# Kernel optimization log

Measured on AMD Instinct MI355X. Metric: run time of the kernel, lower is better.

Reference implementation:

```python
import jax, jax.numpy as jnp
import numpy as np

D_MODEL = 1024
NUM_HEADS = 16
D_K = D_MODEL // NUM_HEADS


def setup_inputs() -> dict:
    key = jax.random.key(0)
    ks = jax.random.split(key, 9)
    B, S = 2, 2048
    s = 1.0 / np.sqrt(D_MODEL)
    return {
        "x": jax.random.normal(ks[0], (B, S, D_MODEL), dtype=jnp.float32),
        "Wq": jax.random.normal(ks[1], (D_MODEL, D_MODEL), dtype=jnp.float32) * s,
        "bq": jnp.zeros((D_MODEL,), dtype=jnp.float32),
        "Wk": jax.random.normal(ks[2], (D_MODEL, D_MODEL), dtype=jnp.float32) * s,
        "bk": jnp.zeros((D_MODEL,), dtype=jnp.float32),
        "Wv": jax.random.normal(ks[3], (D_MODEL, D_MODEL), dtype=jnp.float32) * s,
        "bv": jnp.zeros((D_MODEL,), dtype=jnp.float32),
        "Wo": jax.random.normal(ks[4], (D_MODEL, D_MODEL), dtype=jnp.float32) * s,
        "bo": jnp.zeros((D_MODEL,), dtype=jnp.float32),
    }


def reference(x, Wq, bq, Wk, bk, Wv, bv, Wo, bo):
    B, S, _ = x.shape
    # project and split heads: [B, H, S, d_k]
    def proj(W, b):
        return (x @ W + b).reshape(B, S, NUM_HEADS, D_K).transpose(0, 2, 1, 3)
    Q, K, V = proj(Wq, bq), proj(Wk, bk), proj(Wv, bv)
    scores = jnp.einsum("bhqd,bhkd->bhqk", Q, K) / jnp.sqrt(jnp.float32(D_K))
    causal = jnp.tril(jnp.ones((S, S), dtype=bool))
    scores = jnp.where(causal[None, None], scores, jnp.float32(-1e9))
    attn = jax.nn.softmax(scores, axis=-1)  # dropout=0 (eval)
    out = jnp.einsum("bhqk,bhkd->bhqd", attn, V)
    out = out.transpose(0, 2, 1, 3).reshape(B, S, D_MODEL)
    return out @ Wo + bo
```

## Files before the change

kernel.cpp:

```cpp
#include <hip/hip_runtime.h>

#define SEQ    2048
#define NH     16
#define DMODEL 1024

typedef __attribute__((ext_vector_type(4)))  float f32x4;
typedef __attribute__((ext_vector_type(8)))  short s16x8;
typedef __attribute__((ext_vector_type(4)))  short s16x4;
typedef __attribute__((ext_vector_type(2)))  unsigned u32x2;

__device__ __forceinline__ float bf2f(unsigned short u){
  union { unsigned int i; float f; } v; v.i = ((unsigned int)u) << 16; return v.f;
}
__device__ __forceinline__ unsigned short f2bf(float f){
  union { float f; unsigned int i; } v; v.f = f;
  unsigned int r = v.i + 0x7fffu + ((v.i >> 16) & 1u);
  return (unsigned short)(r >> 16);
}
__device__ __forceinline__ unsigned short f2bf_hu(float f){
  union { float f; unsigned int i; } v; v.f = f;
  return (unsigned short)((v.i + 0x8000u) >> 16);
}
__device__ __forceinline__ float fast_exp2(float x){
  return __builtin_amdgcn_exp2f(x);
}
__device__ __forceinline__ void gld_lds16(const void* g, void* l){
  __builtin_amdgcn_global_load_lds((const __attribute__((address_space(1))) void*)g,
                                   (__attribute__((address_space(3))) void*)l,
                                   16, 0, 0);
}
#define SB() __builtin_amdgcn_sched_barrier(0)

__global__ __launch_bounds__(256) void k_cast_x(const float* __restrict__ x,
                                                unsigned short* __restrict__ hi){
  int i = blockIdx.x * 256 + threadIdx.x;
  f32x4 v = ((const f32x4*)x)[i];
  s16x4 h;
  #pragma unroll
  for (int j = 0; j < 4; ++j) h[j] = (short)f2bf(v[j]);
  ((s16x4*)hi)[i] = h;
}

__global__ __launch_bounds__(256) void k_t_w(const float* __restrict__ W0,
                                             const float* __restrict__ W1,
                                             const float* __restrict__ W2,
                                             const float* __restrict__ W3,
                                             unsigned short* __restrict__ Wt){
  __shared__ float t[64][65];
  const float* Ws[4] = {W0, W1, W2, W3};
  const float* W = Ws[blockIdx.z];
  const int n0 = blockIdx.x * 64, k0 = blockIdx.y * 64;
  const int tid = threadIdx.x;
  #pragma unroll
  for (int i = 0; i < 16; ++i){
    int e = i * 256 + tid;
    int r = e >> 6, c = e & 63;
    t[r][c] = W[(size_t)(k0 + r) * 1024 + n0 + c];
  }
  __syncthreads();
  size_t base = ((size_t)blockIdx.z << 20);
  #pragma unroll
  for (int i = 0; i < 16; ++i){
    int e = i * 256 + tid;
    int nn = e >> 6, kk = e & 63;
    Wt[base + (size_t)(n0 + nn) * 1024 + k0 + kk] = f2bf(t[kk][nn]);
  }
}

__global__ __launch_bounds__(512, 2)
void gemm_qkv8(const unsigned short* __restrict__ A,
               const unsigned short* __restrict__ B,
               const float* __restrict__ bq, const float* __restrict__ bk,
               const float* __restrict__ bv,
               unsigned short* __restrict__ Qb, unsigned short* __restrict__ Kb,
               unsigned short* __restrict__ Vt)
{
  __shared__ __align__(16) unsigned short lA[2][256 * 64];
  __shared__ __align__(16) unsigned short lB[2][192 * 64];
  const int tid = threadIdx.x;
  const int lane = tid & 63, w = tid >> 6;
  const int wm = w >> 2, wn = w & 3;
  const int lr = lane & 15, lq = lane >> 4;
  const int m0 = blockIdx.y * 256, n0 = blockIdx.x * 192;

  size_t asrc[4]; unsigned adst[4];
  #pragma unroll
  for (int p = 0; p < 4; ++p){
    int c = p * 512 + tid;
    int row = c >> 3, lc = (c & 7) ^ (row & 7);
    asrc[p] = (size_t)(m0 + row) * 1024 + lc * 8;
    adst[p] = c * 8;
  }
  size_t bsrc[3]; unsigned bdst[3];
  #pragma unroll
  for (int p = 0; p < 3; ++p){
    int c = p * 512 + tid;
    int row = c >> 3, lc = (c & 7) ^ (row & 7);
    bsrc[p] = (size_t)(n0 + row) * 1024 + lc * 8;
    bdst[p] = c * 8;
  }
  auto stage = [&](int buf, int k0){
    #pragma unroll
    for (int p = 0; p < 4; ++p) gld_lds16(A + asrc[p] + k0, &lA[buf][adst[p]]);
    #pragma unroll
    for (int p = 0; p < 3; ++p) gld_lds16(B + bsrc[p] + k0, &lB[buf][bdst[p]]);
  };

  const int csw0 = ((0 + lq) ^ (lr & 7)) << 4;
  const int csw1 = ((4 + lq) ^ (lr & 7)) << 4;

  f32x4 acc[8][3];
  #pragma unroll
  for (int i = 0; i < 8; ++i)
    #pragma unroll
    for (int j = 0; j < 3; ++j) acc[i][j] = (f32x4)0.0f;

  stage(0, 0);
  stage(1, 64);
  asm volatile("s_waitcnt vmcnt(7)" ::: "memory");
  SB();
  __builtin_amdgcn_s_barrier();
  SB();

  for (int t = 0; t < 16; ++t){
    const int p = t & 1;
    s16x8 fa[8][2], fb[3][2];
    const char* baseA = (const char*)&lA[p][0];
    const char* baseB = (const char*)&lB[p][0];
    #pragma unroll
    for (int mf = 0; mf < 8; ++mf)
      fa[mf][0] = *(const s16x8*)(baseA + (wm * 128 + mf * 16 + lr) * 128 + csw0);
    #pragma unroll
    for (int nf = 0; nf < 3; ++nf)
      fb[nf][0] = *(const s16x8*)(baseB + (wn * 48 + nf * 16 + lr) * 128 + csw0);
    SB();
    #pragma unroll
    for (int mf = 0; mf < 8; ++mf)
      fa[mf][1] = *(const s16x8*)(baseA + (wm * 128 + mf * 16 + lr) * 128 + csw1);
    #pragma unroll
    for (int nf = 0; nf < 3; ++nf)
      fb[nf][1] = *(const s16x8*)(baseB + (wn * 48 + nf * 16 + lr) * 128 + csw1);
    asm volatile("s_waitcnt lgkmcnt(11)" ::: "memory");
    SB();
    #pragma unroll
    for (int mf = 0; mf < 8; ++mf)
      #pragma unroll
      for (int nf = 0; nf < 3; ++nf)
        acc[mf][nf] = __builtin_amdgcn_mfma_f32_16x16x32_bf16(fa[mf][0], fb[nf][0], acc[mf][nf], 0, 0, 0);
    SB();
    asm volatile("s_waitcnt lgkmcnt(0)" ::: "memory");
    SB();
    __builtin_amdgcn_s_barrier();
    SB();
    if (t + 2 < 16) stage(p, (t + 2) * 64);
    #pragma unroll
    for (int mf = 0; mf < 8; ++mf)
      #pragma unroll
      for (int nf = 0; nf < 3; ++nf)
        acc[mf][nf] = __builtin_amdgcn_mfma_f32_16x16x32_bf16(fa[mf][1], fb[nf][1], acc[mf][nf], 0, 0, 0);
    SB();
    if (t < 14) asm volatile("s_waitcnt vmcnt(7)" ::: "memory");
    else        asm volatile("s_waitcnt vmcnt(0)" ::: "memory");
    SB();
    __builtin_amdgcn_s_barrier();
    SB();
  }

  const int mb = m0 + wm * 128, nb = n0 + wn * 48;
  #pragma unroll
  for (int mf = 0; mf < 8; ++mf){
    int row = mb + mf * 16 + lq * 4;
    #pragma unroll
    for (int nf = 0; nf < 3; ++nf){
      int col = nb + nf * 16 + lr;
      int mat = col >> 10, cm = col & 1023;
      float bs = ((mat == 0) ? bq : (mat == 1) ? bk : bv)[cm];
      if (mat < 2){
        unsigned short* QK = mat ? Kb : Qb;
        #pragma unroll
        for (int r = 0; r < 4; ++r)
          QK[(size_t)(row + r) * 1024 + cm] = f2bf(acc[mf][nf][r] + bs);
      } else {
        int bb = row >> 11, s = row & 2047;
        int h = cm >> 6, d = cm & 63;
        s16x4 pk;
        #pragma unroll
        for (int r = 0; r < 4; ++r) pk[r] = (short)f2bf(acc[mf][nf][r] + bs);
        *(s16x4*)&Vt[(((size_t)(bb * NH + h) * 64 + d) << 11) + s] = pk;
      }
    }
  }
}

__global__ __launch_bounds__(256, 2)
void gemm_o8(const unsigned short* __restrict__ A,
             const unsigned short* __restrict__ B,
             const float* __restrict__ bias,
             float* __restrict__ C)
{
  __shared__ __align__(16) unsigned short lA[2][64 * 64];
  __shared__ __align__(16) unsigned short lB[2][128 * 64];
  const int tid = threadIdx.x;
  const int lane = tid & 63, w = tid >> 6;
  const int wm = w >> 1, wn = w & 1;
  const int lr = lane & 15, lq = lane >> 4;
  const int m0 = blockIdx.y * 64, n0 = blockIdx.x * 128;

  size_t asrc[2]; unsigned adst[2];
  #pragma unroll
  for (int p = 0; p < 2; ++p){
    int c = p * 256 + tid;
    int row = c >> 3, lc = (c & 7) ^ (row & 7);
    asrc[p] = (size_t)(m0 + row) * 1024 + lc * 8;
    adst[p] = c * 8;
  }
  size_t bsrc[4]; unsigned bdst[4];
  #pragma unroll
  for (int p = 0; p < 4; ++p){
    int c = p * 256 + tid;
    int row = c >> 3, lc = (c & 7) ^ (row & 7);
    bsrc[p] = (size_t)(n0 + row) * 1024 + lc * 8;
    bdst[p] = c * 8;
  }
  auto stage = [&](int buf, int k0){
    #pragma unroll
    for (int p = 0; p < 2; ++p) gld_lds16(A + asrc[p] + k0, &lA[buf][adst[p]]);
    #pragma unroll
    for (int p = 0; p < 4; ++p) gld_lds16(B + bsrc[p] + k0, &lB[buf][bdst[p]]);
  };

  const int csw0 = ((0 + lq) ^ (lr & 7)) << 4;
  const int csw1 = ((4 + lq) ^ (lr & 7)) << 4;

  f32x4 acc[2][4];
  #pragma unroll
  for (int i = 0; i < 2; ++i)
    #pragma unroll
    for (int j = 0; j < 4; ++j) acc[i][j] = (f32x4)0.0f;

  stage(0, 0);
  stage(1, 64);
  asm volatile("s_waitcnt vmcnt(6)" ::: "memory");
  SB();
  __builtin_amdgcn_s_barrier();
  SB();

  for (int t = 0; t < 16; ++t){
    const int p = t & 1;
    s16x8 fa[2][2], fb[4][2];
    const char* baseA = (const char*)&lA[p][0];
    const char* baseB = (const char*)&lB[p][0];
    #pragma unroll
    for (int mf = 0; mf < 2; ++mf)
      fa[mf][0] = *(const s16x8*)(baseA + (wm * 32 + mf * 16 + lr) * 128 + csw0);
    #pragma unroll
    for (int nf = 0; nf < 4; ++nf)
      fb[nf][0] = *(const s16x8*)(baseB + (wn * 64 + nf * 16 + lr) * 128 + csw0);
    SB();
    #pragma unroll
    for (int mf = 0; mf < 2; ++mf)
      fa[mf][1] = *(const s16x8*)(baseA + (wm * 32 + mf * 16 + lr) * 128 + csw1);
    #pragma unroll
    for (int nf = 0; nf < 4; ++nf)
      fb[nf][1] = *(const s16x8*)(baseB + (wn * 64 + nf * 16 + lr) * 128 + csw1);
    asm volatile("s_waitcnt lgkmcnt(6)" ::: "memory");
    SB();
    #pragma unroll
    for (int i = 0; i < 2; ++i)
      #pragma unroll
      for (int j = 0; j < 4; ++j)
        acc[i][j] = __builtin_amdgcn_mfma_f32_16x16x32_bf16(fa[i][0], fb[j][0], acc[i][j], 0, 0, 0);
    SB();
    asm volatile("s_waitcnt lgkmcnt(0)" ::: "memory");
    SB();
    __builtin_amdgcn_s_barrier();
    SB();
    if (t + 2 < 16) stage(p, (t + 2) * 64);
    #pragma unroll
    for (int i = 0; i < 2; ++i)
      #pragma unroll
      for (int j = 0; j < 4; ++j)
        acc[i][j] = __builtin_amdgcn_mfma_f32_16x16x32_bf16(fa[i][1], fb[j][1], acc[i][j], 0, 0, 0);
    SB();
    if (t < 14) asm volatile("s_waitcnt vmcnt(6)" ::: "memory");
    else        asm volatile("s_waitcnt vmcnt(0)" ::: "memory");
    SB();
    __builtin_amdgcn_s_barrier();
    SB();
  }

  const int mb = m0 + wm * 32, nb = n0 + wn * 64;
  #pragma unroll
  for (int i = 0; i < 2; ++i){
    int row = mb + i * 16 + lq * 4;
    #pragma unroll
    for (int j = 0; j < 4; ++j){
      int col = nb + j * 16 + lr;
      float bs = bias[col];
      #pragma unroll
      for (int r = 0; r < 4; ++r)
        C[(size_t)(row + r) * 1024 + col] = acc[i][j][r] + bs;
    }
  }
}

__global__ __launch_bounds__(256, 4)
void attn_fwd(const unsigned short* __restrict__ Qg,
              const unsigned short* __restrict__ Kg,
              const unsigned short* __restrict__ Vtg,
              unsigned short* __restrict__ Oh)
{
  __shared__ __align__(16) unsigned short lK[2][64 * 64];
  __shared__ __align__(16) unsigned short lV[2][64 * 64];
  __shared__ __align__(16) unsigned short lP[4][16 * 64];
  const int tid = threadIdx.x;
  const int lane = tid & 63, w = tid >> 6;
  const int lr = lane & 15, lq = lane >> 4;
  const int bh = blockIdx.x;
  const int b = bh >> 4, h = bh & 15;
  const int qt = 31 - blockIdx.y;
  const int qrow = qt * 64 + w * 16;

  const float qscale = 0.125f * 1.44269504088896f;
  const float FIXMAX = 11.0f;

  const unsigned short* qp = Qg + (size_t)(b * SEQ + qrow + lr) * 1024 + h * 64 + lq * 8;
  s16x8 q0 = *(const s16x8*)qp;
  s16x8 q1 = *(const s16x8*)(qp + 32);
  #pragma unroll
  for (int j = 0; j < 8; ++j){
    q0[j] = (short)f2bf(bf2f((unsigned short)q0[j]) * qscale);
    q1[j] = (short)f2bf(bf2f((unsigned short)q1[j]) * qscale);
  }

  float ls = 0.f;
  f32x4 accO[4];
  #pragma unroll
  for (int dt = 0; dt < 4; ++dt) accO[dt] = (f32x4)0.0f;

  auto stage = [&](int buf, int kt){
    const int kc0 = kt * 64;
    #pragma unroll
    for (int it = 0; it < 2; ++it){
      int c = it * 256 + tid;
      int row = c >> 3, sc = c & 7;
      int lc = sc ^ (row & 7);
      gld_lds16(Kg + (size_t)(b * SEQ + kc0 + row) * 1024 + h * 64 + lc * 8, &lK[buf][c * 8]);
      gld_lds16(Vtg + ((size_t)(bh * 64 + row) << 11) + kc0 + lc * 8, &lV[buf][c * 8]);
    }
  };

  stage(0, 0);
  if (qt > 0){
    stage(1, 1);
    asm volatile("s_waitcnt vmcnt(4)" ::: "memory");
  } else {
    asm volatile("s_waitcnt vmcnt(0)" ::: "memory");
  }
  SB();
  __builtin_amdgcn_s_barrier();
  SB();

  for (int kt = 0; kt <= qt; ++kt){
    const int cur = kt & 1;
    const bool diag = (kt == qt);

    s16x8 kf[4][2], vf[4][2];
    #pragma unroll
    for (int st = 0; st < 4; ++st){
      int tok = st * 16 + lr;
      const char* kb = (const char*)&lK[cur][0] + tok * 128;
      kf[st][0] = *(const s16x8*)(kb + (((0 + lq) ^ (tok & 7)) << 4));
      kf[st][1] = *(const s16x8*)(kb + (((4 + lq) ^ (tok & 7)) << 4));
    }
    SB();
    #pragma unroll
    for (int st = 0; st < 4; ++st){
      int tok = st * 16 + lr;
      const char* vb = (const char*)&lV[cur][0] + tok * 128;
      vf[st][0] = *(const s16x8*)(vb + (((0 + lq) ^ (tok & 7)) << 4));
      vf[st][1] = *(const s16x8*)(vb + (((4 + lq) ^ (tok & 7)) << 4));
    }
    asm volatile("s_waitcnt lgkmcnt(8)" ::: "memory");
    SB();

    f32x4 s4[4];
    #pragma unroll
    for (int st = 0; st < 4; ++st){
      if (diag && st > w){ s4[st] = (f32x4)(-1e30f); continue; }
      f32x4 z = (f32x4)0.0f;
      z = __builtin_amdgcn_mfma_f32_16x16x32_bf16(kf[st][0], q0, z, 0, 0, 0);
      z = __builtin_amdgcn_mfma_f32_16x16x32_bf16(kf[st][1], q1, z, 0, 0, 0);
      if (diag && st == w){
        #pragma unroll
        for (int r = 0; r < 4; ++r)
          if (lq * 4 + r > lr) z[r] = -1e30f;
      }
      s4[st] = z;
    }
    SB();
    asm volatile("s_waitcnt lgkmcnt(0)" ::: "memory");
    SB();
    __builtin_amdgcn_s_barrier();
    SB();
    if (kt + 2 <= qt) stage(cur, kt + 2);

    char* pb = (char*)&lP[w][0];
    #pragma unroll
    for (int st = 0; st < 4; ++st){
      float p0 = fast_exp2(s4[st][0] - FIXMAX);
      float p1 = fast_exp2(s4[st][1] - FIXMAX);
      float p2 = fast_exp2(s4[st][2] - FIXMAX);
      float p3 = fast_exp2(s4[st][3] - FIXMAX);
      ls += (p0 + p1) + (p2 + p3);
      u32x2 d;
      d[0] = ((unsigned)f2bf_hu(p1) << 16) | f2bf_hu(p0);
      d[1] = ((unsigned)f2bf_hu(p3) << 16) | f2bf_hu(p2);
      int base = lr * 128 + ((st * 32 + lq * 8) ^ ((lr & 7) << 4));
      *(u32x2*)(pb + base) = d;
    }
    asm volatile("s_waitcnt lgkmcnt(0)" ::: "memory");
    SB();
    s16x8 pf0 = *(const s16x8*)(pb + lr * 128 + (((0 + lq) << 4) ^ ((lr & 7) << 4)));
    s16x8 pf1 = *(const s16x8*)(pb + lr * 128 + (((4 + lq) << 4) ^ ((lr & 7) << 4)));

    #pragma unroll
    for (int dt = 0; dt < 4; ++dt){
      accO[dt] = __builtin_amdgcn_mfma_f32_16x16x32_bf16(pf0, vf[dt][0], accO[dt], 0, 0, 0);
      accO[dt] = __builtin_amdgcn_mfma_f32_16x16x32_bf16(pf1, vf[dt][1], accO[dt], 0, 0, 0);
    }
    SB();
    if (kt + 2 <= qt)      asm volatile("s_waitcnt vmcnt(4)" ::: "memory");
    else if (kt + 1 <= qt) asm volatile("s_waitcnt vmcnt(0)" ::: "memory");
    SB();
    __builtin_amdgcn_s_barrier();
    SB();
  }

  float t = ls;
  t += __shfl_xor(t, 16);
  t += __shfl_xor(t, 32);
  #pragma unroll
  for (int r = 0; r < 4; ++r){
    float rn = 1.0f / __shfl(t, lq * 4 + r);
    #pragma unroll
    for (int dt = 0; dt < 4; ++dt){
      size_t off = (size_t)(b * SEQ + qrow + lq * 4 + r) * 1024 + h * 64 + dt * 16 + lr;
      Oh[off] = f2bf(accO[dt][r] * rn);
    }
  }
}

extern "C" void kernel_launch(void* const* d_in, const int* in_sizes, int n_in,
                              void* d_out, int out_size, void* d_ws, size_t ws_size,
                              hipStream_t stream){
  (void)in_sizes; (void)n_in; (void)out_size; (void)ws_size;
  const float* x  = (const float*)d_in[0];
  const float* Wq = (const float*)d_in[1];
  const float* bq = (const float*)d_in[2];
  const float* Wk = (const float*)d_in[3];
  const float* bk = (const float*)d_in[4];
  const float* Wv = (const float*)d_in[5];
  const float* bv = (const float*)d_in[6];
  const float* Wo = (const float*)d_in[7];
  const float* bo = (const float*)d_in[8];

  const size_t NT = 4096;
  unsigned short* xh  = (unsigned short*)d_ws;
  unsigned short* wt  = xh + NT * 1024;
  unsigned short* Qb  = wt + 4u * 1024 * 1024;
  unsigned short* Kb  = Qb + NT * 1024;
  unsigned short* Vt  = Kb + NT * 1024;
  unsigned short* Ohb = Vt + NT * 1024;

  k_cast_x<<<4096, 256, 0, stream>>>(x, xh);
  k_t_w<<<dim3(16, 16, 4), 256, 0, stream>>>(Wq, Wk, Wv, Wo, wt);

  gemm_qkv8<<<dim3(16, 16), 512, 0, stream>>>(xh, wt, bq, bk, bv, Qb, Kb, Vt);

  attn_fwd<<<dim3(32, 32), 256, 0, stream>>>(Qb, Kb, Vt, Ohb);

  const size_t WM = (size_t)1024 * 1024;
  gemm_o8<<<dim3(8, 64), 256, 0, stream>>>(Ohb, wt + 3 * WM, bo, (float*)d_out);
}
```

Baseline: 99.47 us.

## Merge prep kernels into one launch and swizzle GEMM block order per XCD

The x cast kernel and the weight transpose/cast kernel become one launch, with a block-index split choosing which job each block does. This removes one kernel launch and the gap between the two. The QKV and output-projection GEMMs also remap their flat block index so that blocks placed round-robin on the same XCD get neighbouring output tiles, which should improve L2 reuse of the A and B tiles. The remapping has to stay a bijection over the grid; both appear to be valid permutations for the 256-block and 512-block grids.

```diff
diff --git a/kernel.cpp b/kernel.cpp
--- a/kernel.cpp
+++ b/kernel.cpp
@@ -31,39 +31,42 @@
 }
 #define SB() __builtin_amdgcn_sched_barrier(0)
 
-__global__ __launch_bounds__(256) void k_cast_x(const float* __restrict__ x,
-                                                unsigned short* __restrict__ hi){
-  int i = blockIdx.x * 256 + threadIdx.x;
-  f32x4 v = ((const f32x4*)x)[i];
-  s16x4 h;
-  #pragma unroll
-  for (int j = 0; j < 4; ++j) h[j] = (short)f2bf(v[j]);
-  ((s16x4*)hi)[i] = h;
-}
-
-__global__ __launch_bounds__(256) void k_t_w(const float* __restrict__ W0,
-                                             const float* __restrict__ W1,
-                                             const float* __restrict__ W2,
-                                             const float* __restrict__ W3,
-                                             unsigned short* __restrict__ Wt){
+__global__ __launch_bounds__(256) void k_prep(const float* __restrict__ x,
+                                              const float* __restrict__ W0,
+                                              const float* __restrict__ W1,
+                                              const float* __restrict__ W2,
+                                              const float* __restrict__ W3,
+                                              unsigned short* __restrict__ Wt,
+                                              unsigned short* __restrict__ xh){
   __shared__ float t[64][65];
-  const float* Ws[4] = {W0, W1, W2, W3};
-  const float* W = Ws[blockIdx.z];
-  const int n0 = blockIdx.x * 64, k0 = blockIdx.y * 64;
+  const int bid = blockIdx.x;
   const int tid = threadIdx.x;
-  #pragma unroll
-  for (int i = 0; i < 16; ++i){
-    int e = i * 256 + tid;
-    int r = e >> 6, c = e & 63;
-    t[r][c] = W[(size_t)(k0 + r) * 1024 + n0 + c];
-  }
-  __syncthreads();
-  size_t base = ((size_t)blockIdx.z << 20);
-  #pragma unroll
-  for (int i = 0; i < 16; ++i){
-    int e = i * 256 + tid;
-    int nn = e >> 6, kk = e & 63;
-    Wt[base + (size_t)(n0 + nn) * 1024 + k0 + kk] = f2bf(t[kk][nn]);
+  if (bid < 1024){
+    const int z = bid >> 8, rem = bid & 255;
+    const int n0 = (rem & 15) * 64, k0 = (rem >> 4) * 64;
+    const float* Ws[4] = {W0, W1, W2, W3};
+    const float* W = Ws[z];
+    #pragma unroll
+    for (int i = 0; i < 16; ++i){
+      int e = i * 256 + tid;
+      int r = e >> 6, c = e & 63;
+      t[r][c] = W[(size_t)(k0 + r) * 1024 + n0 + c];
+    }
+    __syncthreads();
+    size_t base = ((size_t)z << 20);
+    #pragma unroll
+    for (int i = 0; i < 16; ++i){
+      int e = i * 256 + tid;
+      int nn = e >> 6, kk = e & 63;
+      Wt[base + (size_t)(n0 + nn) * 1024 + k0 + kk] = f2bf(t[kk][nn]);
+    }
+  } else {
+    int i = (bid - 1024) * 256 + tid;
+    f32x4 v = ((const f32x4*)x)[i];
+    s16x4 h;
+    #pragma unroll
+    for (int j = 0; j < 4; ++j) h[j] = (short)f2bf(v[j]);
+    ((s16x4*)xh)[i] = h;
   }
 }
 
@@ -81,7 +84,9 @@
   const int lane = tid & 63, w = tid >> 6;
   const int wm = w >> 2, wn = w & 3;
   const int lr = lane & 15, lq = lane >> 4;
-  const int m0 = blockIdx.y * 256, n0 = blockIdx.x * 192;
+  const int wg  = blockIdx.x + blockIdx.y * 16;
+  const int swz = (wg & 7) * 32 + (wg >> 3);
+  const int m0 = (swz >> 4) * 256, n0 = (swz & 15) * 192;
 
   size_t asrc[4]; unsigned adst[4];
   #pragma unroll
@@ -204,7 +209,9 @@
   const int lane = tid & 63, w = tid >> 6;
   const int wm = w >> 1, wn = w & 1;
   const int lr = lane & 15, lq = lane >> 4;
-  const int m0 = blockIdx.y * 64, n0 = blockIdx.x * 128;
+  const int wg  = blockIdx.x + blockIdx.y * 8;
+  const int swz = (wg & 7) * 64 + (wg >> 3);
+  const int m0 = (swz >> 3) * 64, n0 = (swz & 7) * 128;
 
   size_t asrc[2]; unsigned adst[2];
   #pragma unroll
@@ -473,8 +480,7 @@
   unsigned short* Vt  = Kb + NT * 1024;
   unsigned short* Ohb = Vt + NT * 1024;
 
-  k_cast_x<<<4096, 256, 0, stream>>>(x, xh);
-  k_t_w<<<dim3(16, 16, 4), 256, 0, stream>>>(Wq, Wk, Wv, Wo, wt);
+  k_prep<<<5120, 256, 0, stream>>>(x, Wq, Wk, Wv, Wo, wt, xh);
 
   gemm_qkv8<<<dim3(16, 16), 512, 0, stream>>>(xh, wt, bq, bk, bv, Qb, Kb, Vt);
 
```

New measurement: 96.08 us, median of 2. 3.4% less time.
